# Optimization experiments

Measured on AMD Instinct MI355X. Metric: run time of the kernel, lower is better.

## Reference

```python
import jax, jax.numpy as jnp
import numpy as np

H = 128          # hidden size
D = 2048         # input size
B, T = 64, 256   # batch, seq_len


def _lstm_layer(x_proj, Whh, h0, c0):
    """x_proj: [B,T,4H] precomputed input projection (+ both biases).
    Returns (full hidden sequence [B,T,H], final hidden [B,H]).
    PyTorch gate order: i, f, g, o."""
    def step(carry, xt):
        h, c = carry
        g = xt + h @ Whh.T                      # [B,4H]
        i, f, gg, o = jnp.split(g, 4, axis=-1)
        i = jax.nn.sigmoid(i)
        f = jax.nn.sigmoid(f)
        gg = jnp.tanh(gg)
        o = jax.nn.sigmoid(o)
        c = f * c + i * gg
        h = o * jnp.tanh(c)
        return (h, c), h

    (hT, _), hs = jax.lax.scan(step, (h0, c0), jnp.swapaxes(x_proj, 0, 1))
    return jnp.swapaxes(hs, 0, 1), hT


def setup_inputs() -> dict:
    key = jax.random.key(0)
    ks = jax.random.split(key, 11)
    k = 1.0 / np.sqrt(H)  # torch default init bound
    u = lambda kk, shape: jax.random.uniform(kk, shape, jnp.float32, -k, k)
    return {
        "x":    jax.random.normal(ks[0], (B, T, D), jnp.float32),
        "Wih0": u(ks[1], (4 * H, D)),
        "Whh0": u(ks[2], (4 * H, H)),
        "bih0": u(ks[3], (4 * H,)),
        "bhh0": u(ks[4], (4 * H,)),
        "Wih1": u(ks[5], (4 * H, H)),
        "Whh1": u(ks[6], (4 * H, H)),
        "bih1": u(ks[7], (4 * H,)),
        "bhh1": u(ks[8], (4 * H,)),
        "Wfc":  u(ks[9], (1, H)),
        "bfc":  u(ks[10], (1,)),
    }


def reference(x, Wih0, Whh0, bih0, bhh0, Wih1, Whh1, bih1, bhh1, Wfc, bfc):
    b = x.shape[0]
    h0 = jnp.zeros((b, H), x.dtype)
    # layer 0: batch the big input GEMM across all timesteps
    xp0 = jnp.einsum('btd,gd->btg', x, Wih0) + bih0 + bhh0   # [B,T,4H]
    seq0, _ = _lstm_layer(xp0, Whh0, h0, h0)
    # layer 1 (dropout disabled in eval)
    xp1 = jnp.einsum('bth,gh->btg', seq0, Wih1) + bih1 + bhh1
    _, hT = _lstm_layer(xp1, Whh1, h0, h0)                   # h_n[-1]
    return hT @ Wfc.T + bfc                                  # [B,1]
```

## Files before the change

kernel.cpp:

```cpp
#include <hip/hip_runtime.h>
#include <math.h>

#define HH 128
#define DD 2048
#define BATCH 64
#define TT 256
#define G4 512

#define BM 128
#define BN 128
#define TK 16
#define GT 256

__global__ __launch_bounds__(GT) void gemm_bias_nt(
    const float* __restrict__ A, const float* __restrict__ Bw,
    const float* __restrict__ b1, const float* __restrict__ b2,
    float* __restrict__ C, int M, int N, int K)
{
    __shared__ float As[TK][BM + 4];
    __shared__ float Bs[TK][BN + 4];

    const int tid = threadIdx.x;
    const int tx = tid & 15;
    const int ty = tid >> 4;
    const int r  = tid >> 2;
    const int kq = (tid & 3) << 2;

    const float* Ab = A  + (size_t)blockIdx.x * BM * K;
    const float* Bb = Bw + (size_t)blockIdx.y * BN * K;

    float acc[8][8];
#pragma unroll
    for (int i = 0; i < 8; ++i)
#pragma unroll
        for (int j = 0; j < 8; ++j) acc[i][j] = 0.f;

    for (int k0 = 0; k0 < K; k0 += TK) {
        float4 a0  = *(const float4*)(Ab + (size_t)r        * K + k0 + kq);
        float4 a1  = *(const float4*)(Ab + (size_t)(r + 64) * K + k0 + kq);
        float4 b0  = *(const float4*)(Bb + (size_t)r        * K + k0 + kq);
        float4 b1v = *(const float4*)(Bb + (size_t)(r + 64) * K + k0 + kq);
        __syncthreads();
        As[kq+0][r]    = a0.x;  As[kq+1][r]    = a0.y;  As[kq+2][r]    = a0.z;  As[kq+3][r]    = a0.w;
        As[kq+0][r+64] = a1.x;  As[kq+1][r+64] = a1.y;  As[kq+2][r+64] = a1.z;  As[kq+3][r+64] = a1.w;
        Bs[kq+0][r]    = b0.x;  Bs[kq+1][r]    = b0.y;  Bs[kq+2][r]    = b0.z;  Bs[kq+3][r]    = b0.w;
        Bs[kq+0][r+64] = b1v.x; Bs[kq+1][r+64] = b1v.y; Bs[kq+2][r+64] = b1v.z; Bs[kq+3][r+64] = b1v.w;
        __syncthreads();

#pragma unroll
        for (int k = 0; k < TK; ++k) {
            float4 av0 = *(const float4*)&As[k][ty * 4];
            float4 av1 = *(const float4*)&As[k][64 + ty * 4];
            float4 bv0 = *(const float4*)&Bs[k][tx * 4];
            float4 bv1 = *(const float4*)&Bs[k][64 + tx * 4];
            float a[8] = {av0.x, av0.y, av0.z, av0.w, av1.x, av1.y, av1.z, av1.w};
            float b[8] = {bv0.x, bv0.y, bv0.z, bv0.w, bv1.x, bv1.y, bv1.z, bv1.w};
#pragma unroll
            for (int i = 0; i < 8; ++i)
#pragma unroll
                for (int j = 0; j < 8; ++j)
                    acc[i][j] = fmaf(a[i], b[j], acc[i][j]);
        }
    }

#pragma unroll
    for (int i = 0; i < 8; ++i) {
        int row = blockIdx.x * BM + ((i < 4) ? (ty * 4 + i) : (64 + ty * 4 + (i - 4)));
        float* crow = C + (size_t)row * N + blockIdx.y * BN;
#pragma unroll
        for (int j = 0; j < 8; ++j) {
            int col = (j < 4) ? (tx * 4 + j) : (64 + tx * 4 + (j - 4));
            int gcol = blockIdx.y * BN + col;
            crow[col] = acc[i][j] + b1[gcol] + b2[gcol];
        }
    }
}

template <bool WRITE_SEQ, bool FINAL_FC>
__global__ __launch_bounds__(512) void lstm_rec(
    const float* __restrict__ xp,
    const float* __restrict__ Whh,
    float* __restrict__ seq_out,
    const float* __restrict__ Wfc,
    const float* __restrict__ bfc,
    float* __restrict__ out)
{
    const int b = blockIdx.x;
    const int j = threadIdx.x;

    __shared__ float h_lds[HH];
    __shared__ float g_lds[G4];

    float w[HH];
#pragma unroll
    for (int q = 0; q < 32; ++q) {
        float4 t4 = *(const float4*)(Whh + (size_t)j * HH + q * 4);
        w[4*q+0] = t4.x; w[4*q+1] = t4.y; w[4*q+2] = t4.z; w[4*q+3] = t4.w;
    }

    if (j < HH) h_lds[j] = 0.f;
    float c = 0.f;
    __syncthreads();

    const float* xprow = xp + (size_t)b * TT * G4 + j;
    float xt = xprow[0];

    for (int t = 0; t < TT; ++t) {
        int tn = (t + 1 < TT) ? (t + 1) : (TT - 1);
        float xt_next = xprow[(size_t)tn * G4];

        float s0 = xt, s1 = 0.f, s2 = 0.f, s3 = 0.f;
#pragma unroll
        for (int q = 0; q < 32; ++q) {
            float4 hv = *(const float4*)&h_lds[q * 4];
            s0 = fmaf(w[4*q+0], hv.x, s0);
            s1 = fmaf(w[4*q+1], hv.y, s1);
            s2 = fmaf(w[4*q+2], hv.z, s2);
            s3 = fmaf(w[4*q+3], hv.w, s3);
        }
        float g = (s0 + s1) + (s2 + s3);

        const int gt = j >> 7;
        float act = (gt == 2) ? tanhf(g) : (1.f / (1.f + expf(-g)));
        g_lds[j] = act;
        __syncthreads();

        if (j < HH) {
            float iv = g_lds[j];
            float fv = g_lds[HH + j];
            float gv = g_lds[2 * HH + j];
            float ov = g_lds[3 * HH + j];
            c = fmaf(fv, c, iv * gv);
            float h = ov * tanhf(c);
            h_lds[j] = h;
            if (WRITE_SEQ)
                seq_out[(size_t)b * TT * HH + (size_t)t * HH + j] = h;
        }
        __syncthreads();
        xt = xt_next;
    }

    if (FINAL_FC) {
        if (j < 64) {
            float p = h_lds[j] * Wfc[j] + h_lds[j + 64] * Wfc[j + 64];
#pragma unroll
            for (int off = 32; off > 0; off >>= 1)
                p += __shfl_down(p, off, 64);
            if (j == 0) out[b] = p + bfc[0];
        }
    }
}

extern "C" void kernel_launch(void* const* d_in, const int* in_sizes, int n_in,
                              void* d_out, int out_size, void* d_ws, size_t ws_size,
                              hipStream_t stream)
{
    const float* x    = (const float*)d_in[0];
    const float* Wih0 = (const float*)d_in[1];
    const float* Whh0 = (const float*)d_in[2];
    const float* bih0 = (const float*)d_in[3];
    const float* bhh0 = (const float*)d_in[4];
    const float* Wih1 = (const float*)d_in[5];
    const float* Whh1 = (const float*)d_in[6];
    const float* bih1 = (const float*)d_in[7];
    const float* bhh1 = (const float*)d_in[8];
    const float* Wfc  = (const float*)d_in[9];
    const float* bfc  = (const float*)d_in[10];
    float* out = (float*)d_out;

    const int M = BATCH * TT;
    float* xp  = (float*)d_ws;
    float* seq = xp + (size_t)M * G4;

    gemm_bias_nt<<<dim3(M / BM, G4 / BN), GT, 0, stream>>>(
        x, Wih0, bih0, bhh0, xp, M, G4, DD);

    lstm_rec<true, false><<<BATCH, 512, 0, stream>>>(
        xp, Whh0, seq, nullptr, nullptr, nullptr);

    gemm_bias_nt<<<dim3(M / BM, G4 / BN), GT, 0, stream>>>(
        seq, Wih1, bih1, bhh1, xp, M, G4, HH);

    lstm_rec<false, true><<<BATCH, 512, 0, stream>>>(
        xp, Whh1, nullptr, Wfc, bfc, out);
}
```

Measured before the change: 1.076 ms.

## Use split-bf16 MFMA GEMM and fp16-dot LSTM recurrence with fast activations

The input-projection GEMM moves from scalar FP32 FMAs to MFMA bf16 instructions, with each operand split into high and low bf16 parts and three MFMAs per tile to keep near-FP32 accuracy. The recurrent kernel drops to 128 threads per batch row. Each thread computes all four gates for one hidden unit using fp16 weights held in registers and fdot2, and uses a double-buffered fp16 h so there is one barrier per step instead of two. Sigmoid and tanh switch to exp2/rcp intrinsics. The fp16 recurrent weights and state lower precision, and holding 256 weight registers per thread risks spills and low occupancy.

```diff
diff --git a/kernel.cpp b/kernel.cpp
--- a/kernel.cpp
+++ b/kernel.cpp
@@ -7,77 +7,145 @@
 #define TT 256
 #define G4 512
 
-#define BM 128
-#define BN 128
-#define TK 16
-#define GT 256
-
-__global__ __launch_bounds__(GT) void gemm_bias_nt(
+typedef __attribute__((ext_vector_type(8))) short bf16x8;
+typedef __attribute__((ext_vector_type(4))) float f32x4;
+typedef _Float16 h2 __attribute__((ext_vector_type(2)));
+
+static __device__ __forceinline__ unsigned short f2bf_rne(float f) {
+    union { float f; unsigned u; } v; v.f = f;
+    unsigned r = v.u + 0x7fff + ((v.u >> 16) & 1);
+    return (unsigned short)(r >> 16);
+}
+static __device__ __forceinline__ float bf2f(unsigned short b) {
+    union { unsigned u; float f; } v; v.u = ((unsigned)b) << 16;
+    return v.f;
+}
+static __device__ __forceinline__ float fdot2f(h2 a, h2 b, float c) {
+#if __has_builtin(__builtin_amdgcn_fdot2)
+    return __builtin_amdgcn_fdot2(a, b, c, false);
+#else
+    return fmaf((float)a[0], (float)b[0], fmaf((float)a[1], (float)b[1], c));
+#endif
+}
+static __device__ __forceinline__ float fexp2(float x) {
+#if __has_builtin(__builtin_amdgcn_exp2f)
+    return __builtin_amdgcn_exp2f(x);
+#else
+    return exp2f(x);
+#endif
+}
+static __device__ __forceinline__ float frcp(float x) {
+#if __has_builtin(__builtin_amdgcn_rcpf)
+    return __builtin_amdgcn_rcpf(x);
+#else
+    return 1.f / x;
+#endif
+}
+static __device__ __forceinline__ float sigmoid_f(float x) {
+    return frcp(1.f + fexp2(-1.44269504f * x));
+}
+static __device__ __forceinline__ float tanh_f(float x) {
+    float xx = fminf(fmaxf(x, -15.f), 15.f);
+    float e = fexp2(2.88539008f * xx);
+    return 1.f - 2.f * frcp(e + 1.f);
+}
+
+#define PK 40
+
+__global__ __launch_bounds__(256) void gemm_split_bf16(
     const float* __restrict__ A, const float* __restrict__ Bw,
     const float* __restrict__ b1, const float* __restrict__ b2,
     float* __restrict__ C, int M, int N, int K)
 {
-    __shared__ float As[TK][BM + 4];
-    __shared__ float Bs[TK][BN + 4];
+    __shared__ unsigned short Ah[128 * PK], Al[128 * PK];
+    __shared__ unsigned short Bh[128 * PK], Bl[128 * PK];
 
     const int tid = threadIdx.x;
-    const int tx = tid & 15;
-    const int ty = tid >> 4;
-    const int r  = tid >> 2;
-    const int kq = (tid & 3) << 2;
-
-    const float* Ab = A  + (size_t)blockIdx.x * BM * K;
-    const float* Bb = Bw + (size_t)blockIdx.y * BN * K;
-
-    float acc[8][8];
-#pragma unroll
-    for (int i = 0; i < 8; ++i)
-#pragma unroll
-        for (int j = 0; j < 8; ++j) acc[i][j] = 0.f;
-
-    for (int k0 = 0; k0 < K; k0 += TK) {
-        float4 a0  = *(const float4*)(Ab + (size_t)r        * K + k0 + kq);
-        float4 a1  = *(const float4*)(Ab + (size_t)(r + 64) * K + k0 + kq);
-        float4 b0  = *(const float4*)(Bb + (size_t)r        * K + k0 + kq);
-        float4 b1v = *(const float4*)(Bb + (size_t)(r + 64) * K + k0 + kq);
-        __syncthreads();
-        As[kq+0][r]    = a0.x;  As[kq+1][r]    = a0.y;  As[kq+2][r]    = a0.z;  As[kq+3][r]    = a0.w;
-        As[kq+0][r+64] = a1.x;  As[kq+1][r+64] = a1.y;  As[kq+2][r+64] = a1.z;  As[kq+3][r+64] = a1.w;
-        Bs[kq+0][r]    = b0.x;  Bs[kq+1][r]    = b0.y;  Bs[kq+2][r]    = b0.z;  Bs[kq+3][r]    = b0.w;
-        Bs[kq+0][r+64] = b1v.x; Bs[kq+1][r+64] = b1v.y; Bs[kq+2][r+64] = b1v.z; Bs[kq+3][r+64] = b1v.w;
-        __syncthreads();
-
-#pragma unroll
-        for (int k = 0; k < TK; ++k) {
-            float4 av0 = *(const float4*)&As[k][ty * 4];
-            float4 av1 = *(const float4*)&As[k][64 + ty * 4];
-            float4 bv0 = *(const float4*)&Bs[k][tx * 4];
-            float4 bv1 = *(const float4*)&Bs[k][64 + tx * 4];
-            float a[8] = {av0.x, av0.y, av0.z, av0.w, av1.x, av1.y, av1.z, av1.w};
-            float b[8] = {bv0.x, bv0.y, bv0.z, bv0.w, bv1.x, bv1.y, bv1.z, bv1.w};
-#pragma unroll
-            for (int i = 0; i < 8; ++i)
-#pragma unroll
-                for (int j = 0; j < 8; ++j)
-                    acc[i][j] = fmaf(a[i], b[j], acc[i][j]);
-        }
-    }
-
-#pragma unroll
-    for (int i = 0; i < 8; ++i) {
-        int row = blockIdx.x * BM + ((i < 4) ? (ty * 4 + i) : (64 + ty * 4 + (i - 4)));
-        float* crow = C + (size_t)row * N + blockIdx.y * BN;
-#pragma unroll
-        for (int j = 0; j < 8; ++j) {
-            int col = (j < 4) ? (tx * 4 + j) : (64 + tx * 4 + (j - 4));
-            int gcol = blockIdx.y * BN + col;
-            crow[col] = acc[i][j] + b1[gcol] + b2[gcol];
+    const int l = tid & 63;
+    const int w = tid >> 6;
+    const int wr = w >> 1, wc = w & 1;
+    const int bm = blockIdx.y, bn = blockIdx.x;
+
+    f32x4 acc[4][4];
+#pragma unroll
+    for (int m = 0; m < 4; ++m)
+#pragma unroll
+        for (int n = 0; n < 4; ++n) acc[m][n] = f32x4{0.f, 0.f, 0.f, 0.f};
+
+    const float* Ab = A  + (size_t)(bm * 128) * K;
+    const float* Bb = Bw + (size_t)(bn * 128) * K;
+
+    for (int k0 = 0; k0 < K; k0 += 32) {
+        __syncthreads();
+#pragma unroll
+        for (int q = 0; q < 4; ++q) {
+            int fid = tid + 256 * q;
+            int r = fid >> 3;
+            int kk = (fid & 7) << 2;
+            float4 av = *(const float4*)(Ab + (size_t)r * K + k0 + kk);
+            float4 bv = *(const float4*)(Bb + (size_t)r * K + k0 + kk);
+            float a4[4] = {av.x, av.y, av.z, av.w};
+            float b4[4] = {bv.x, bv.y, bv.z, bv.w};
+            ushort4 ahv, alv, bhv, blv;
+            unsigned short t;
+            t = f2bf_rne(a4[0]); ahv.x = t; alv.x = f2bf_rne(a4[0] - bf2f(t));
+            t = f2bf_rne(a4[1]); ahv.y = t; alv.y = f2bf_rne(a4[1] - bf2f(t));
+            t = f2bf_rne(a4[2]); ahv.z = t; alv.z = f2bf_rne(a4[2] - bf2f(t));
+            t = f2bf_rne(a4[3]); ahv.w = t; alv.w = f2bf_rne(a4[3] - bf2f(t));
+            t = f2bf_rne(b4[0]); bhv.x = t; blv.x = f2bf_rne(b4[0] - bf2f(t));
+            t = f2bf_rne(b4[1]); bhv.y = t; blv.y = f2bf_rne(b4[1] - bf2f(t));
+            t = f2bf_rne(b4[2]); bhv.z = t; blv.z = f2bf_rne(b4[2] - bf2f(t));
+            t = f2bf_rne(b4[3]); bhv.w = t; blv.w = f2bf_rne(b4[3] - bf2f(t));
+            int off = r * PK + kk;
+            *(ushort4*)&Ah[off] = ahv;
+            *(ushort4*)&Al[off] = alv;
+            *(ushort4*)&Bh[off] = bhv;
+            *(ushort4*)&Bl[off] = blv;
+        }
+        __syncthreads();
+
+        bf16x8 aH[4], aL[4], bH[4], bL[4];
+#pragma unroll
+        for (int m = 0; m < 4; ++m) {
+            int row = wr * 64 + m * 16 + (l & 15);
+            int off = row * PK + 8 * (l >> 4);
+            aH[m] = *(const bf16x8*)&Ah[off];
+            aL[m] = *(const bf16x8*)&Al[off];
+        }
+#pragma unroll
+        for (int n = 0; n < 4; ++n) {
+            int row = wc * 64 + n * 16 + (l & 15);
+            int off = row * PK + 8 * (l >> 4);
+            bH[n] = *(const bf16x8*)&Bh[off];
+            bL[n] = *(const bf16x8*)&Bl[off];
+        }
+#pragma unroll
+        for (int m = 0; m < 4; ++m)
+#pragma unroll
+            for (int n = 0; n < 4; ++n) {
+                acc[m][n] = __builtin_amdgcn_mfma_f32_16x16x32_bf16(aH[m], bH[n], acc[m][n], 0, 0, 0);
+                acc[m][n] = __builtin_amdgcn_mfma_f32_16x16x32_bf16(aH[m], bL[n], acc[m][n], 0, 0, 0);
+                acc[m][n] = __builtin_amdgcn_mfma_f32_16x16x32_bf16(aL[m], bH[n], acc[m][n], 0, 0, 0);
+            }
+    }
+
+#pragma unroll
+    for (int n = 0; n < 4; ++n) {
+        int cg = bn * 128 + wc * 64 + n * 16 + (l & 15);
+        float bias = b1[cg] + b2[cg];
+#pragma unroll
+        for (int m = 0; m < 4; ++m) {
+            int r0 = bm * 128 + wr * 64 + m * 16 + ((l >> 4) << 2);
+            f32x4 v = acc[m][n];
+#pragma unroll
+            for (int i = 0; i < 4; ++i)
+                C[(size_t)(r0 + i) * N + cg] = v[i] + bias;
         }
     }
 }
 
 template <bool WRITE_SEQ, bool FINAL_FC>
-__global__ __launch_bounds__(512) void lstm_rec(
+__global__ __launch_bounds__(128, 1) void lstm_rec_f16(
     const float* __restrict__ xp,
     const float* __restrict__ Whh,
     float* __restrict__ seq_out,
@@ -88,66 +156,73 @@
     const int b = blockIdx.x;
     const int j = threadIdx.x;
 
-    __shared__ float h_lds[HH];
-    __shared__ float g_lds[G4];
-
-    float w[HH];
-#pragma unroll
-    for (int q = 0; q < 32; ++q) {
-        float4 t4 = *(const float4*)(Whh + (size_t)j * HH + q * 4);
-        w[4*q+0] = t4.x; w[4*q+1] = t4.y; w[4*q+2] = t4.z; w[4*q+3] = t4.w;
-    }
-
-    if (j < HH) h_lds[j] = 0.f;
-    float c = 0.f;
+    __shared__ alignas(16) _Float16 hbuf[2][HH];
+    __shared__ float red[2];
+
+    h2 wreg[4][64];
+#pragma unroll
+    for (int g = 0; g < 4; ++g) {
+        const float4* wrow = (const float4*)(Whh + (size_t)(g * HH + j) * HH);
+#pragma unroll
+        for (int q = 0; q < 32; ++q) {
+            float4 t = wrow[q];
+            wreg[g][2 * q]     = h2{(_Float16)t.x, (_Float16)t.y};
+            wreg[g][2 * q + 1] = h2{(_Float16)t.z, (_Float16)t.w};
+        }
+    }
+
+    hbuf[0][j] = (_Float16)0.f;
+    float c = 0.f, hlast = 0.f;
+
+    const float* xb = xp + (size_t)b * TT * G4;
+    float xi = xb[j], xf = xb[HH + j], xg = xb[2 * HH + j], xo = xb[3 * HH + j];
     __syncthreads();
 
-    const float* xprow = xp + (size_t)b * TT * G4 + j;
-    float xt = xprow[0];
-
+    int cur = 0;
     for (int t = 0; t < TT; ++t) {
-        int tn = (t + 1 < TT) ? (t + 1) : (TT - 1);
-        float xt_next = xprow[(size_t)tn * G4];
-
-        float s0 = xt, s1 = 0.f, s2 = 0.f, s3 = 0.f;
-#pragma unroll
-        for (int q = 0; q < 32; ++q) {
-            float4 hv = *(const float4*)&h_lds[q * 4];
-            s0 = fmaf(w[4*q+0], hv.x, s0);
-            s1 = fmaf(w[4*q+1], hv.y, s1);
-            s2 = fmaf(w[4*q+2], hv.z, s2);
-            s3 = fmaf(w[4*q+3], hv.w, s3);
-        }
-        float g = (s0 + s1) + (s2 + s3);
-
-        const int gt = j >> 7;
-        float act = (gt == 2) ? tanhf(g) : (1.f / (1.f + expf(-g)));
-        g_lds[j] = act;
-        __syncthreads();
-
-        if (j < HH) {
-            float iv = g_lds[j];
-            float fv = g_lds[HH + j];
-            float gv = g_lds[2 * HH + j];
-            float ov = g_lds[3 * HH + j];
-            c = fmaf(fv, c, iv * gv);
-            float h = ov * tanhf(c);
-            h_lds[j] = h;
-            if (WRITE_SEQ)
-                seq_out[(size_t)b * TT * HH + (size_t)t * HH + j] = h;
-        }
-        __syncthreads();
-        xt = xt_next;
+        const float* xn = xb + (size_t)(t + 1 < TT ? t + 1 : t) * G4;
+        float ni = xn[j], nf = xn[HH + j], ng = xn[2 * HH + j], no = xn[3 * HH + j];
+
+        float ai = xi, af = xf, ag = xg, ao = xo;
+        const uint4* hp = (const uint4*)&hbuf[cur][0];
+#pragma unroll
+        for (int q = 0; q < 16; ++q) {
+            uint4 hv = hp[q];
+            union { unsigned u; h2 h; } c0, c1, c2, c3;
+            c0.u = hv.x; c1.u = hv.y; c2.u = hv.z; c3.u = hv.w;
+            ai = fdot2f(wreg[0][4*q+0], c0.h, ai); ai = fdot2f(wreg[0][4*q+1], c1.h, ai);
+            ai = fdot2f(wreg[0][4*q+2], c2.h, ai); ai = fdot2f(wreg[0][4*q+3], c3.h, ai);
+            af = fdot2f(wreg[1][4*q+0], c0.h, af); af = fdot2f(wreg[1][4*q+1], c1.h, af);
+            af = fdot2f(wreg[1][4*q+2], c2.h, af); af = fdot2f(wreg[1][4*q+3], c3.h, af);
+            ag = fdot2f(wreg[2][4*q+0], c0.h, ag); ag = fdot2f(wreg[2][4*q+1], c1.h, ag);
+            ag = fdot2f(wreg[2][4*q+2], c2.h, ag); ag = fdot2f(wreg[2][4*q+3], c3.h, ag);
+            ao = fdot2f(wreg[3][4*q+0], c0.h, ao); ao = fdot2f(wreg[3][4*q+1], c1.h, ao);
+            ao = fdot2f(wreg[3][4*q+2], c2.h, ao); ao = fdot2f(wreg[3][4*q+3], c3.h, ao);
+        }
+
+        float iv = sigmoid_f(ai);
+        float fv = sigmoid_f(af);
+        float ov = sigmoid_f(ao);
+        float gv = tanh_f(ag);
+        c = fmaf(fv, c, iv * gv);
+        float h = ov * tanh_f(c);
+
+        hbuf[cur ^ 1][j] = (_Float16)h;
+        if (WRITE_SEQ)
+            seq_out[((size_t)b * TT + t) * HH + j] = h;
+        hlast = h;
+        __syncthreads();
+        cur ^= 1;
+        xi = ni; xf = nf; xg = ng; xo = no;
     }
 
     if (FINAL_FC) {
-        if (j < 64) {
-            float p = h_lds[j] * Wfc[j] + h_lds[j + 64] * Wfc[j + 64];
-#pragma unroll
-            for (int off = 32; off > 0; off >>= 1)
-                p += __shfl_down(p, off, 64);
-            if (j == 0) out[b] = p + bfc[0];
-        }
+        float p = hlast * Wfc[j];
+#pragma unroll
+        for (int off = 32; off > 0; off >>= 1) p += __shfl_down(p, off, 64);
+        if ((j & 63) == 0) red[j >> 6] = p;
+        __syncthreads();
+        if (j == 0) out[b] = red[0] + red[1] + bfc[0];
     }
 }
 
@@ -172,15 +247,15 @@
     float* xp  = (float*)d_ws;
     float* seq = xp + (size_t)M * G4;
 
-    gemm_bias_nt<<<dim3(M / BM, G4 / BN), GT, 0, stream>>>(
+    gemm_split_bf16<<<dim3(G4 / 128, M / 128), 256, 0, stream>>>(
         x, Wih0, bih0, bhh0, xp, M, G4, DD);
 
-    lstm_rec<true, false><<<BATCH, 512, 0, stream>>>(
+    lstm_rec_f16<true, false><<<BATCH, HH, 0, stream>>>(
         xp, Whh0, seq, nullptr, nullptr, nullptr);
 
-    gemm_bias_nt<<<dim3(M / BM, G4 / BN), GT, 0, stream>>>(
+    gemm_split_bf16<<<dim3(G4 / 128, M / 128), 256, 0, stream>>>(
         seq, Wih1, bih1, bhh1, xp, M, G4, HH);
 
-    lstm_rec<false, true><<<BATCH, 512, 0, stream>>>(
+    lstm_rec_f16<false, true><<<BATCH, HH, 0, stream>>>(
         xp, Whh1, nullptr, Wfc, bfc, out);
 }
```

Measured after the change: 991.7 us. 1.09x faster.
